# Optimization experiments

Hardware: AMD Instinct MI355X
Metric: run time of the kernel (lower is better)

Reference implementation:

```python
import jax, jax.numpy as jnp
import numpy as np

N = 100000
E = 1600000
F_IN = 64
HID = 64
OUT = 64


def _sage_conv(x, src, dst, w_l, b_l, w_r):
    # PyG SAGEConv (mean aggr): out = lin_l(mean_{j in N(i)} x_j) + lin_r(x_i)
    msgs = x[src]                                             # [E, F] gather
    summed = jax.ops.segment_sum(msgs, dst, num_segments=N)   # [N, F]
    ones = jnp.ones((src.shape[0],), dtype=x.dtype)
    cnt = jax.ops.segment_sum(ones, dst, num_segments=N)      # [N]
    mean = summed / jnp.maximum(cnt, 1.0)[:, None]
    return mean @ w_l + b_l + x @ w_r


def setup_inputs() -> dict:
    key = jax.random.key(0)
    ks = jax.random.split(key, 12)
    sc = lambda f: 1.0 / np.sqrt(f)
    inp = {
        "h": jax.random.normal(ks[0], (N, F_IN), dtype=jnp.float32),
        "edge_index": jax.random.randint(ks[1], (2, E), 0, N, dtype=jnp.int64),
        # conv1: lin_l (with bias) and lin_r (no bias), weights stored [in, out]
        "w1_l": jax.random.normal(ks[2], (F_IN, HID), dtype=jnp.float32) * sc(F_IN),
        "b1_l": jnp.zeros((HID,), dtype=jnp.float32),
        "w1_r": jax.random.normal(ks[3], (F_IN, HID), dtype=jnp.float32) * sc(F_IN),
        "w_lin1": jax.random.normal(ks[4], (HID, HID), dtype=jnp.float32) * sc(HID),
        "b_lin1": jnp.zeros((HID,), dtype=jnp.float32),
        "w2_l": jax.random.normal(ks[5], (HID, HID), dtype=jnp.float32) * sc(HID),
        "b2_l": jnp.zeros((HID,), dtype=jnp.float32),
        "w2_r": jax.random.normal(ks[6], (HID, HID), dtype=jnp.float32) * sc(HID),
        "w_lin2": jax.random.normal(ks[7], (HID, OUT), dtype=jnp.float32) * sc(HID),
        "b_lin2": jnp.zeros((OUT,), dtype=jnp.float32),
    }
    return inp


def reference(h, edge_index, w1_l, b1_l, w1_r, w_lin1, b_lin1,
              w2_l, b2_l, w2_r, w_lin2, b_lin2):
    src, dst = edge_index[0], edge_index[1]
    x = jax.nn.relu(_sage_conv(h, src, dst, w1_l, b1_l, w1_r))
    x = jax.nn.relu(x @ w_lin1 + b_lin1)
    x = jax.nn.relu(_sage_conv(x, src, dst, w2_l, b2_l, w2_r))
    x = x @ w_lin2 + b_lin2
    return x
```

## Files before the change

### kernel.cpp

```cpp
#include <hip/hip_runtime.h>
#include <hip/hip_fp16.h>

#define FEAT   64
#define BSHIFT 8
#define BNODES 256
#define MAXB   512
#define CHUNK  4096
#define REGION 5120

typedef _Float16 half8 __attribute__((ext_vector_type(8)));
typedef float  float4v __attribute__((ext_vector_type(4)));

__global__ __launch_bounds__(256) void setup_kernel(
    const float* __restrict__ h, __half* __restrict__ h16, int n4, int CB,
    const float* w0, const float* w1, const float* w2,
    const float* w3, const float* w4, const float* w5,
    __half* __restrict__ wT, int* __restrict__ bcur)
{
    int b = blockIdx.x;
    if (b < CB) {
        int i = b * 256 + threadIdx.x;
        if (i < n4) {
            float4 v = ((const float4*)h)[i];
            union { uint2 u; __half2 h2[2]; } r;
            r.h2[0] = __floats2half2_rn(v.x, v.y);
            r.h2[1] = __floats2half2_rn(v.z, v.w);
            ((uint2*)h16)[i] = r.u;
        }
    } else if (b < CB + 96) {
        int bb = b - CB;
        int m = bb >> 4;
        int idx = ((bb & 15) << 8) | threadIdx.x;
        const float* src = m==0?w0 : m==1?w1 : m==2?w2 : m==3?w3 : m==4?w4 : w5;
        int o = idx >> 6, i = idx & 63;
        wT[m * 4096 + o * 64 + i] = __float2half(src[i * 64 + o]);
    } else {
        bcur[threadIdx.x] = 0;
        bcur[threadIdx.x + 256] = 0;
    }
}

__global__ __launch_bounds__(512) void partition_kernel(
    const int* __restrict__ src, const int* __restrict__ dst,
    int* __restrict__ bcur, int* __restrict__ pedge, int E)
{
    __shared__ int cnt[MAXB];
    __shared__ int sa[MAXB], sb[MAXB];
    __shared__ int gb[MAXB];
    __shared__ int lcur[MAXB];
    __shared__ int stage[CHUNK];
    __shared__ int tgt[CHUNK];

    int tid = threadIdx.x;
    cnt[tid] = 0;
    __syncthreads();

    int base = blockIdx.x * CHUNK;
    int vals[8];
    int bs[8];
#pragma unroll
    for (int i = 0; i < 8; i++) {
        int e = base + tid + i * 512;
        bs[i] = -1;
        if (e < E) {
            int s_ = src[e];
            int d_ = dst[e];
            int b  = d_ >> BSHIFT;
            bs[i]  = b;
            vals[i] = s_ | ((d_ & (BNODES - 1)) << 20);
            atomicAdd(&cnt[b], 1);
        }
    }
    __syncthreads();

    sa[tid] = cnt[tid];
    __syncthreads();
    int* cur = sa; int* nxt = sb;
    for (int off = 1; off < MAXB; off <<= 1) {
        nxt[tid] = cur[tid] + ((tid >= off) ? cur[tid - off] : 0);
        __syncthreads();
        int* tmp = cur; cur = nxt; nxt = tmp;
    }
    {
        int c = cnt[tid];
        int lo = cur[tid] - c;
        int gbase = c ? atomicAdd(&bcur[tid], c) : 0;
        if (gbase > REGION) gbase = REGION;
        gb[tid]   = tid * REGION + gbase - lo;
        lcur[tid] = lo;
    }
    __syncthreads();

#pragma unroll
    for (int i = 0; i < 8; i++) {
        if (bs[i] >= 0) {
            int pos = atomicAdd(&lcur[bs[i]], 1);
            stage[pos] = vals[i];
            tgt[pos]   = gb[bs[i]];
        }
    }
    __syncthreads();

    int cn = min(CHUNK, E - base);
    for (int i = tid; i < cn; i += 512)
        pedge[tgt[i] + i] = stage[i];
}

__global__ __launch_bounds__(512) void buildcsr_kernel(
    const int* __restrict__ pedge, const int* __restrict__ bcur,
    unsigned* __restrict__ rowinfo, int* __restrict__ csr, int N)
{
    __shared__ int stg[REGION];
    __shared__ int srt[REGION];
    __shared__ int hist[BNODES], scn[BNODES], lcur[BNODES];
    int b = blockIdx.x;
    int tid = threadIdx.x;
    int beg = b * REGION;
    int cnt = min(bcur[b], REGION);

    if (tid < BNODES) hist[tid] = 0;
    __syncthreads();

    for (int i = tid; i < cnt; i += 512) {
        int p = pedge[beg + i];
        stg[i] = p;
        atomicAdd(&hist[p >> 20], 1);
    }
    __syncthreads();

    int v = 0;
    if (tid < BNODES) { v = hist[tid]; scn[tid] = v; }
    __syncthreads();
    for (int off = 1; off < BNODES; off <<= 1) {
        int t = 0;
        if (tid < BNODES && tid >= off) t = scn[tid - off];
        __syncthreads();
        if (tid < BNODES) scn[tid] += t;
        __syncthreads();
    }
    if (tid < BNODES) {
        int excl = scn[tid] - v;
        int node = (b << BSHIFT) + tid;
        if (node < N)
            rowinfo[node] = (unsigned)(beg + excl) | ((unsigned)v << 21);
        lcur[tid] = excl;
    }
    __syncthreads();

    for (int i = tid; i < cnt; i += 512) {
        int p = stg[i];
        int pos = atomicAdd(&lcur[p >> 20], 1);
        srt[pos] = p & 0xFFFFF;
    }
    __syncthreads();
    for (int i = tid; i < cnt; i += 512)
        csr[beg + i] = srt[i];
}

__global__ __launch_bounds__(256) void fused_layer_kernel(
    const __half* __restrict__ x, const unsigned* __restrict__ rowinfo,
    const int* __restrict__ csr_src,
    const __half* __restrict__ wlT, const __half* __restrict__ wrT,
    const __half* __restrict__ w2T,
    const float* __restrict__ b1, const float* __restrict__ b2,
    float* __restrict__ out_f, __half* __restrict__ out_h,
    int n, int relu_out)
{
    __shared__ __attribute__((aligned(16))) _Float16 sbuf[64][72];

    int tid  = threadIdx.x;
    int wave = tid >> 6;
    int lane = tid & 63;
    int sg   = tid >> 4;
    int gg   = (tid >> 3) & 1;
    int s8   = tid & 7;
    int r    = lane & 15;
    int q    = lane >> 4;
    int base = blockIdx.x * 64 + wave * 16;

    int arow = min(base + r, n - 1);
    const half8* xrow = (const half8*)(x + (size_t)arow * FEAT);
    half8 Ax0 = xrow[q], Ax1 = xrow[4 + q];

    unsigned infos[4];
#pragma unroll
    for (int i = 0; i < 4; i++) {
        int node = blockIdx.x * 64 + sg * 4 + i;
        infos[i] = (node < n) ? rowinfo[node] : 0u;
    }

#pragma unroll
    for (int i = 0; i < 4; i++) {
        int beg = (int)(infos[i] & 0x1FFFFFu);
        int deg = (int)(infos[i] >> 21);
        int end = beg + deg;
        float acc[8] = {0.f,0.f,0.f,0.f,0.f,0.f,0.f,0.f};
        int e = beg + gg;
        for (; e + 2 < end; e += 4) {
            int i0 = csr_src[e];
            int i1 = csr_src[e + 2];
            union { uint4 u; __half2 h2[4]; } r0, r1;
            r0.u = ((const uint4*)(x + (size_t)i0 * FEAT))[s8];
            r1.u = ((const uint4*)(x + (size_t)i1 * FEAT))[s8];
#pragma unroll
            for (int t = 0; t < 4; t++) {
                float2 f0 = __half22float2(r0.h2[t]);
                float2 f1 = __half22float2(r1.h2[t]);
                acc[2*t]   += f0.x + f1.x;
                acc[2*t+1] += f0.y + f1.y;
            }
        }
        if (e < end) {
            int i0 = csr_src[e];
            union { uint4 u; __half2 h2[4]; } r0;
            r0.u = ((const uint4*)(x + (size_t)i0 * FEAT))[s8];
#pragma unroll
            for (int t = 0; t < 4; t++) {
                float2 f0 = __half22float2(r0.h2[t]);
                acc[2*t]   += f0.x;
                acc[2*t+1] += f0.y;
            }
        }
#pragma unroll
        for (int t = 0; t < 8; t++)
            acc[t] += __shfl_xor(acc[t], 8, 64);
        if (gg == 0) {
            float inv = deg ? 1.0f / (float)deg : 0.0f;
            union { uint4 u; __half2 h2[4]; } o;
            o.h2[0] = __floats2half2_rn(acc[0]*inv, acc[1]*inv);
            o.h2[1] = __floats2half2_rn(acc[2]*inv, acc[3]*inv);
            o.h2[2] = __floats2half2_rn(acc[4]*inv, acc[5]*inv);
            o.h2[3] = __floats2half2_rn(acc[6]*inv, acc[7]*inv);
            int ln = sg * 4 + i;
            *(uint4*)&sbuf[ln][s8 * 8] = o.u;
        }
    }
    __syncthreads();

    union { uint4 u4; half8 h; } Am0u, Am1u;
    Am0u.u4 = *(const uint4*)&sbuf[wave * 16 + r][q * 8];
    Am1u.u4 = *(const uint4*)&sbuf[wave * 16 + r][(4 + q) * 8];

    float4v acc1[4];
#pragma unroll
    for (int c = 0; c < 4; c++) {
        float bv = b1[c * 16 + r];
        acc1[c] = (float4v){bv, bv, bv, bv};
        const half8* bl = (const half8*)(wlT + (size_t)(c * 16 + r) * FEAT);
        const half8* br = (const half8*)(wrT + (size_t)(c * 16 + r) * FEAT);
        acc1[c] = __builtin_amdgcn_mfma_f32_16x16x32_f16(Am0u.h, bl[q],     acc1[c], 0, 0, 0);
        acc1[c] = __builtin_amdgcn_mfma_f32_16x16x32_f16(Am1u.h, bl[4 + q], acc1[c], 0, 0, 0);
        acc1[c] = __builtin_amdgcn_mfma_f32_16x16x32_f16(Ax0,    br[q],     acc1[c], 0, 0, 0);
        acc1[c] = __builtin_amdgcn_mfma_f32_16x16x32_f16(Ax1,    br[4 + q], acc1[c], 0, 0, 0);
    }
#pragma unroll
    for (int c = 0; c < 4; c++)
#pragma unroll
        for (int t = 0; t < 4; t++)
            sbuf[wave * 16 + q * 4 + t][c * 16 + r] = (_Float16)fmaxf(acc1[c][t], 0.0f);
    __syncthreads();

    union { uint4 u4; half8 h; } A2[2];
#pragma unroll
    for (int s = 0; s < 2; s++)
        A2[s].u4 = *(const uint4*)&sbuf[wave * 16 + r][s * 32 + q * 8];

    float4v acc2[4];
#pragma unroll
    for (int c = 0; c < 4; c++) {
        float bv = b2[c * 16 + r];
        acc2[c] = (float4v){bv, bv, bv, bv};
        const half8* bw = (const half8*)(w2T + (size_t)(c * 16 + r) * FEAT);
        acc2[c] = __builtin_amdgcn_mfma_f32_16x16x32_f16(A2[0].h, bw[q],     acc2[c], 0, 0, 0);
        acc2[c] = __builtin_amdgcn_mfma_f32_16x16x32_f16(A2[1].h, bw[4 + q], acc2[c], 0, 0, 0);
    }

#pragma unroll
    for (int c = 0; c < 4; c++)
#pragma unroll
        for (int t = 0; t < 4; t++) {
            int gr = base + q * 4 + t;
            if (gr < n) {
                float v = acc2[c][t];
                if (relu_out) v = fmaxf(v, 0.0f);
                if (out_h) out_h[(size_t)gr * FEAT + c * 16 + r] = __float2half(v);
                else       out_f[(size_t)gr * FEAT + c * 16 + r] = v;
            }
        }
}

extern "C" void kernel_launch(void* const* d_in, const int* in_sizes, int n_in,
                              void* d_out, int out_size, void* d_ws, size_t ws_size,
                              hipStream_t stream) {
    const float* h      = (const float*)d_in[0];
    const int*   ei     = (const int*)d_in[1];
    const float* w1_l   = (const float*)d_in[2];
    const float* b1_l   = (const float*)d_in[3];
    const float* w1_r   = (const float*)d_in[4];
    const float* w_lin1 = (const float*)d_in[5];
    const float* b_lin1 = (const float*)d_in[6];
    const float* w2_l   = (const float*)d_in[7];
    const float* b2_l   = (const float*)d_in[8];
    const float* w2_r   = (const float*)d_in[9];
    const float* w_lin2 = (const float*)d_in[10];
    const float* b_lin2 = (const float*)d_in[11];

    const int N = in_sizes[0] / FEAT;
    const int E = in_sizes[1] / 2;
    const int* src  = ei;
    const int* dst_ = ei + E;

    const int NB = (N + BNODES - 1) >> BSHIFT;
    const int PB = (E + CHUNK - 1) / CHUNK;
    const int n4 = N * FEAT / 4;
    const int CB = (n4 + 255) / 256;
    const int fblk = (N + 63) / 64;

    size_t off = 0;
    int* bcur       = (int*)d_ws + off; off += MAXB;
    unsigned* rowinfo = (unsigned*)((int*)d_ws + off); off += (size_t)N;
    off = (off + 3) & ~(size_t)3;
    int* csr    = (int*)d_ws + off; off += (size_t)NB * REGION + 64;
    off = (off + 3) & ~(size_t)3;
    __half* h16 = (__half*)((int*)d_ws + off); off += (size_t)N * FEAT / 2;
    __half* x2h = (__half*)((int*)d_ws + off); off += (size_t)N * FEAT / 2;
    __half* wT  = (__half*)((int*)d_ws + off); off += 6 * 2048;
    int* pedge  = (int*)d_ws + off; off += (size_t)NB * REGION;

    setup_kernel<<<CB + 96 + 1, 256, 0, stream>>>(
        h, h16, n4, CB, w1_l, w1_r, w_lin1, w2_l, w2_r, w_lin2, wT, bcur);
    partition_kernel<<<PB, 512, 0, stream>>>(src, dst_, bcur, pedge, E);
    buildcsr_kernel<<<NB, 512, 0, stream>>>(pedge, bcur, rowinfo, csr, N);

    fused_layer_kernel<<<fblk, 256, 0, stream>>>(
        h16, rowinfo, csr,
        wT + 0 * 4096, wT + 1 * 4096, wT + 2 * 4096,
        b1_l, b_lin1, (float*)nullptr, x2h, N, 1);

    fused_layer_kernel<<<fblk, 256, 0, stream>>>(
        x2h, rowinfo, csr,
        wT + 3 * 4096, wT + 4 * 4096, wT + 5 * 4096,
        b2_l, b_lin2, (float*)d_out, (__half*)nullptr, N, 0);
}
```

Before: 249.7 us.

## Interleave gathers across four nodes with predicated loads and prefetched indices

```diff
diff --git a/kernel.cpp b/kernel.cpp
--- a/kernel.cpp
+++ b/kernel.cpp
@@ -189,48 +189,84 @@
         infos[i] = (node < n) ? rowinfo[node] : 0u;
     }
 
+    int beg4[4], deg4[4];
+    int itmax = 0;
 #pragma unroll
     for (int i = 0; i < 4; i++) {
-        int beg = (int)(infos[i] & 0x1FFFFFu);
-        int deg = (int)(infos[i] >> 21);
-        int end = beg + deg;
-        float acc[8] = {0.f,0.f,0.f,0.f,0.f,0.f,0.f,0.f};
-        int e = beg + gg;
-        for (; e + 2 < end; e += 4) {
-            int i0 = csr_src[e];
-            int i1 = csr_src[e + 2];
+        beg4[i] = (int)(infos[i] & 0x1FFFFFu);
+        deg4[i] = (int)(infos[i] >> 21);
+        int it = (deg4[i] + 3) >> 2;
+        itmax = max(itmax, it);
+    }
+    float acc[4][8];
+#pragma unroll
+    for (int i = 0; i < 4; i++)
+#pragma unroll
+        for (int t = 0; t < 8; t++) acc[i][t] = 0.f;
+
+    int  c0[4], c1[4];
+    bool p0[4], p1[4];
+#pragma unroll
+    for (int i = 0; i < 4; i++) {
+        int be = beg4[i] + gg;
+        int en = beg4[i] + deg4[i];
+        p0[i] = be < en;
+        p1[i] = be + 2 < en;
+        c0[i] = csr_src[p0[i] ? be : beg4[i]];
+        c1[i] = csr_src[p1[i] ? be + 2 : beg4[i]];
+    }
+
+    for (int it = 0; it < itmax; ++it) {
+        int  n0[4], n1[4];
+        bool m0[4], m1[4];
+#pragma unroll
+        for (int i = 0; i < 4; i++) {
+            int be = beg4[i] + gg + (it + 1) * 4;
+            int en = beg4[i] + deg4[i];
+            m0[i] = be < en;
+            m1[i] = be + 2 < en;
+            n0[i] = csr_src[m0[i] ? be : beg4[i]];
+            n1[i] = csr_src[m1[i] ? be + 2 : beg4[i]];
+        }
+#pragma unroll
+        for (int i = 0; i < 4; i++) {
+            int j0 = p0[i] ? c0[i] : 0;
+            int j1 = p1[i] ? c1[i] : 0;
             union { uint4 u; __half2 h2[4]; } r0, r1;
-            r0.u = ((const uint4*)(x + (size_t)i0 * FEAT))[s8];
-            r1.u = ((const uint4*)(x + (size_t)i1 * FEAT))[s8];
+            r0.u = ((const uint4*)(x + (size_t)j0 * FEAT))[s8];
+            r1.u = ((const uint4*)(x + (size_t)j1 * FEAT))[s8];
+            float w0 = p0[i] ? 1.0f : 0.0f;
+            float w1 = p1[i] ? 1.0f : 0.0f;
 #pragma unroll
             for (int t = 0; t < 4; t++) {
                 float2 f0 = __half22float2(r0.h2[t]);
                 float2 f1 = __half22float2(r1.h2[t]);
-                acc[2*t]   += f0.x + f1.x;
-                acc[2*t+1] += f0.y + f1.y;
+                acc[i][2*t]   = fmaf(w0, f0.x, acc[i][2*t]);
+                acc[i][2*t]   = fmaf(w1, f1.x, acc[i][2*t]);
+                acc[i][2*t+1] = fmaf(w0, f0.y, acc[i][2*t+1]);
+                acc[i][2*t+1] = fmaf(w1, f1.y, acc[i][2*t+1]);
             }
         }
-        if (e < end) {
-            int i0 = csr_src[e];
-            union { uint4 u; __half2 h2[4]; } r0;
-            r0.u = ((const uint4*)(x + (size_t)i0 * FEAT))[s8];
-#pragma unroll
-            for (int t = 0; t < 4; t++) {
-                float2 f0 = __half22float2(r0.h2[t]);
-                acc[2*t]   += f0.x;
-                acc[2*t+1] += f0.y;
-            }
-        }
+#pragma unroll
+        for (int i = 0; i < 4; i++) {
+            c0[i] = n0[i]; c1[i] = n1[i];
+            p0[i] = m0[i]; p1[i] = m1[i];
+        }
+    }
+
+#pragma unroll
+    for (int i = 0; i < 4; i++) {
 #pragma unroll
         for (int t = 0; t < 8; t++)
-            acc[t] += __shfl_xor(acc[t], 8, 64);
+            acc[i][t] += __shfl_xor(acc[i][t], 8, 64);
         if (gg == 0) {
+            int deg = deg4[i];
             float inv = deg ? 1.0f / (float)deg : 0.0f;
             union { uint4 u; __half2 h2[4]; } o;
-            o.h2[0] = __floats2half2_rn(acc[0]*inv, acc[1]*inv);
-            o.h2[1] = __floats2half2_rn(acc[2]*inv, acc[3]*inv);
-            o.h2[2] = __floats2half2_rn(acc[4]*inv, acc[5]*inv);
-            o.h2[3] = __floats2half2_rn(acc[6]*inv, acc[7]*inv);
+            o.h2[0] = __floats2half2_rn(acc[i][0]*inv, acc[i][1]*inv);
+            o.h2[1] = __floats2half2_rn(acc[i][2]*inv, acc[i][3]*inv);
+            o.h2[2] = __floats2half2_rn(acc[i][4]*inv, acc[i][5]*inv);
+            o.h2[3] = __floats2half2_rn(acc[i][6]*inv, acc[i][7]*inv);
             int ln = sg * 4 + i;
             *(uint4*)&sbuf[ln][s8 * 8] = o.u;
         }
```

Measured after the change: 235.0 us. 5.9% less time.
